# Performance work log

Hardware: AMD Instinct MI355X
Metric: run time of the kernel (lower is better)

## Reference

```python
import jax, jax.numpy as jnp
import numpy as np

SIGMA = 0.3
EPS = 1e-8  # torch CosineSimilarity eps
LOG_SQRT_2PI = float(0.5 * np.log(2.0 * np.pi))


def setup_inputs() -> dict:
    key = jax.random.key(0)
    k1, k2 = jax.random.split(key)
    Ex = jax.random.normal(k1, (8192, 256), dtype=jnp.float32)
    Ey = jax.random.normal(k2, (8192, 256), dtype=jnp.float32)
    return {"Ex": Ex, "Ey": Ey}


def reference(Ex, Ey):
    # cosine similarity: normalize rows (clamped norms), then dot -> [n, m]
    xn = Ex / jnp.maximum(jnp.linalg.norm(Ex, axis=-1, keepdims=True), EPS)
    yn = Ey / jnp.maximum(jnp.linalg.norm(Ey, axis=-1, keepdims=True), EPS)
    M = jnp.einsum('nd,md->nm', xn, yn)
    # Normal(loc=1, scale=sigma).log_prob
    z = (M - 1.0) / SIGMA
    logp = -0.5 * z * z - jnp.log(jnp.asarray(SIGMA, M.dtype)) - LOG_SQRT_2PI
    # C = -(exp(logp) * logp); row-wise min over y-tokens -> [n]
    C = -jnp.exp(logp) * logp
    return jnp.min(C, axis=-1)
```

## Files before the change

kernel.cpp:

```cpp
#include <hip/hip_runtime.h>
#include <hip/hip_bf16.h>

typedef unsigned short u16;
typedef __attribute__((ext_vector_type(8))) short short8;
typedef __attribute__((ext_vector_type(4))) float floatx4;

#define NROWS 8192
#define DIM 256

__device__ __forceinline__ void atomicMinFloat(float* addr, float val) {
    if (val >= 0.0f) {
        atomicMin((int*)addr, __float_as_int(val));
    } else {
        atomicMax((unsigned int*)addr, __float_as_uint(val));
    }
}

__device__ __forceinline__ u16 f32_to_bf16_rne(float x) {
    unsigned int u = __float_as_uint(x);
    unsigned int r = (u + 0x7fffu + ((u >> 16) & 1u)) >> 16;
    return (u16)r;
}

__device__ __forceinline__ float c_of_m(float m) {
    const float INV_SIG = 1.0f / 0.3f;
    const float KC = 0.28503427f;
    float z = (m - 1.0f) * INV_SIG;
    float logp = fmaf(-0.5f * z, z, KC);
    return -logp * __expf(logp);
}

__device__ __forceinline__ void load16(const u16* g, u16* l) {
    __builtin_amdgcn_global_load_lds(
        (__attribute__((address_space(1))) void*)g,
        (__attribute__((address_space(3))) void*)l, 16, 0, 0);
}

__global__ __launch_bounds__(256) void normalize_kernel(const float* __restrict__ Ex,
                                                        const float* __restrict__ Ey,
                                                        u16* __restrict__ Xs,
                                                        u16* __restrict__ Ys,
                                                        float* __restrict__ out) {
    const int t = threadIdx.x;
    const int ln = t & 63;
    const int row = blockIdx.x * 4 + (t >> 6);
    const float* src = (blockIdx.y == 0) ? Ex : Ey;
    u16* dst = (blockIdx.y == 0) ? Xs : Ys;

    float4 v = *(const float4*)(src + (size_t)row * DIM + ln * 4);
    float s = fmaf(v.x, v.x, fmaf(v.y, v.y, fmaf(v.z, v.z, v.w * v.w)));
    #pragma unroll
    for (int m = 32; m >= 1; m >>= 1) s += __shfl_xor(s, m, 64);
    float inv = 1.0f / fmaxf(sqrtf(s), 1e-8f);

    ushort4 o;
    o.x = f32_to_bf16_rne(v.x * inv);
    o.y = f32_to_bf16_rne(v.y * inv);
    o.z = f32_to_bf16_rne(v.z * inv);
    o.w = f32_to_bf16_rne(v.w * inv);

    const int p = row >> 4;
    const int lm = row & 15;
    const int kt = ln >> 3;
    const int lq = (ln >> 1) & 3;
    const int j4 = (ln & 1) * 4;
    const size_t off = ((size_t)((p * 8 + kt) * 64 + lq * 16 + lm)) * 8 + j4;
    *(ushort4*)(dst + off) = o;

    if (blockIdx.y == 0 && ln == 0) out[row] = __uint_as_float(0x7f800000u);
}

__global__ void __launch_bounds__(512, 2)
gemm_min_kernel(const u16* __restrict__ Xs,
                const u16* __restrict__ Ys,
                float* __restrict__ out) {
    __shared__ u16 Bs[2][16 * 512];

    const int tid = threadIdx.x;
    const int w = tid >> 6;
    const int lane = tid & 63;
    const int lq = lane >> 4;
    const int lm = lane & 15;

    const int i = blockIdx.x;
    const int x = i & 7;
    const int jj = i >> 3;
    const int rt = (x & 3) * 4 + (jj & 3);
    const int cgrp = (x >> 2) * 8 + (jj >> 2);

    const int rowStart = rt * 512;
    const int rowPan0 = rt * 32 + w * 4;
    const u16* ybase = Ys + (size_t)cgrp * 32 * 4096;

    auto stage1 = [&](int buf, const u16* yb, int iu) {
        const int u = w * 2 + iu;
        load16(yb + (u >> 3) * 4096 + (u & 7) * 512 + lane * 8,
               &Bs[buf][u * 512]);
    };

    short8 a[4][8];
    auto loadA = [&](int kt) {
        #pragma unroll
        for (int rg = 0; rg < 4; ++rg)
            a[rg][kt] = *(const short8*)(
                Xs + ((size_t)(rowPan0 + rg) * 8 + kt) * 512 + lane * 8);
    };

    floatx4 mn4[4], mx4[4];
    #pragma unroll
    for (int rg = 0; rg < 4; ++rg) {
        mn4[rg] = (floatx4){3.4e38f, 3.4e38f, 3.4e38f, 3.4e38f};
        mx4[rg] = (floatx4){-3.4e38f, -3.4e38f, -3.4e38f, -3.4e38f};
    }

    floatx4 acc[4][2];
    const floatx4 FZ = (floatx4){0.0f, 0.0f, 0.0f, 0.0f};

    auto compute = [&](int buf) {
        #pragma unroll
        for (int kt = 0; kt < 8; ++kt) {
            short8 bf[2];
            #pragma unroll
            for (int cg = 0; cg < 2; ++cg)
                bf[cg] = *(const short8*)(&Bs[buf][(cg * 8 + kt) * 512 + lane * 8]);
            if (kt == 0) {
                #pragma unroll
                for (int cg = 0; cg < 2; ++cg)
                    #pragma unroll
                    for (int rg = 0; rg < 4; ++rg)
                        acc[rg][cg] = __builtin_amdgcn_mfma_f32_16x16x32_bf16(
                            a[rg][0], bf[cg], FZ, 0, 0, 0);
            } else {
                #pragma unroll
                for (int cg = 0; cg < 2; ++cg)
                    #pragma unroll
                    for (int rg = 0; rg < 4; ++rg)
                        acc[rg][cg] = __builtin_amdgcn_mfma_f32_16x16x32_bf16(
                            a[rg][kt], bf[cg], acc[rg][cg], 0, 0, 0);
            }
        }
    };
    auto fold = [&]() {
        #pragma unroll
        for (int rg = 0; rg < 4; ++rg)
            #pragma unroll
            for (int cg = 0; cg < 2; ++cg)
                #pragma unroll
                for (int r = 0; r < 4; ++r) {
                    float m = acc[rg][cg][r];
                    mn4[rg][r] = fminf(mn4[rg][r], m);
                    mx4[rg][r] = fmaxf(mx4[rg][r], m);
                }
    };

    stage1(0, ybase, 0); stage1(0, ybase, 1);
    loadA(0); loadA(1);
    __syncthreads();
    stage1(1, ybase + 8192, 0); stage1(1, ybase + 8192, 1);
    loadA(2); loadA(3); loadA(4); loadA(5); loadA(6); loadA(7);
    compute(0);
    fold();
    ybase += 8192;

    #pragma unroll 1
    for (int ct = 1; ct < 16; ++ct) {
        const int buf = ct & 1;
        __syncthreads();
        if (ct < 15)
            stage1(buf ^ 1, ybase + 8192, 0), stage1(buf ^ 1, ybase + 8192, 1);
        compute(buf);
        fold();
        ybase += 8192;
    }

    #pragma unroll
    for (int rg = 0; rg < 4; ++rg) {
        #pragma unroll
        for (int r = 0; r < 4; ++r) {
            float mn = mn4[rg][r];
            float mx = mx4[rg][r];
            #pragma unroll
            for (int mofs = 1; mofs < 16; mofs <<= 1) {
                mn = fminf(mn, __shfl_xor(mn, mofs, 64));
                mx = fmaxf(mx, __shfl_xor(mx, mofs, 64));
            }
            if (lm == 0) {
                float cmin = fminf(c_of_m(mn), c_of_m(mx));
                int row = rowStart + w * 64 + rg * 16 + lq * 4 + r;
                atomicMinFloat(&out[row], cmin);
            }
        }
    }
}

extern "C" void kernel_launch(void* const* d_in, const int* in_sizes, int n_in,
                              void* d_out, int out_size, void* d_ws, size_t ws_size,
                              hipStream_t stream) {
    const float* Ex = (const float*)d_in[0];
    const float* Ey = (const float*)d_in[1];
    float* out = (float*)d_out;
    u16* Xs = (u16*)d_ws;
    u16* Ys = Xs + (size_t)NROWS * DIM;

    hipLaunchKernelGGL(normalize_kernel, dim3(NROWS / 4, 2), dim3(256), 0, stream,
                       Ex, Ey, Xs, Ys, out);
    hipLaunchKernelGGL(gemm_min_kernel, dim3(16 * 16), dim3(512), 0, stream,
                       Xs, Ys, out);
}
```

Baseline: 94.52 us.

## Rotate per-wave k-order and software-pipeline LDS B reads across tiles

Each wave now stages the Y k-slices it will consume first and walks the k dimension in a rotated order (w+s), so its first B fragments come from its own global-to-LDS loads. B fragments are double-buffered in registers and read from LDS one step ahead of the MFMAs. The first fragment of the next tile is read before the barrier, right after a vmcnt(0) wait on the wave's own staged loads. The fold of the previous tile's accumulators is moved into the start of the next compute to overlap with the LDS reads. The intent is to hide LDS latency and barrier stalls, at the cost of more registers and a subtle reliance on each wave having staged its own slices.

```diff
diff --git a/kernel.cpp b/kernel.cpp
--- a/kernel.cpp
+++ b/kernel.cpp
@@ -92,17 +92,17 @@
     const int rowPan0 = rt * 32 + w * 4;
     const u16* ybase = Ys + (size_t)cgrp * 32 * 4096;
 
-    auto stage1 = [&](int buf, const u16* yb, int iu) {
-        const int u = w * 2 + iu;
-        load16(yb + (u >> 3) * 4096 + (u & 7) * 512 + lane * 8,
-               &Bs[buf][u * 512]);
+    auto stageOwn = [&](int buf, const u16* yb) {
+        load16(yb + 0 * 4096 + w * 512 + lane * 8, &Bs[buf][(0 * 8 + w) * 512]);
+        load16(yb + 1 * 4096 + w * 512 + lane * 8, &Bs[buf][(8 + w) * 512]);
     };
 
     short8 a[4][8];
-    auto loadA = [&](int kt) {
+    auto loadA = [&](int s) {
+        const int kt = (w + s) & 7;
         #pragma unroll
         for (int rg = 0; rg < 4; ++rg)
-            a[rg][kt] = *(const short8*)(
+            a[rg][s] = *(const short8*)(
                 Xs + ((size_t)(rowPan0 + rg) * 8 + kt) * 512 + lane * 8);
     };
 
@@ -115,31 +115,8 @@
 
     floatx4 acc[4][2];
     const floatx4 FZ = (floatx4){0.0f, 0.0f, 0.0f, 0.0f};
-
-    auto compute = [&](int buf) {
-        #pragma unroll
-        for (int kt = 0; kt < 8; ++kt) {
-            short8 bf[2];
-            #pragma unroll
-            for (int cg = 0; cg < 2; ++cg)
-                bf[cg] = *(const short8*)(&Bs[buf][(cg * 8 + kt) * 512 + lane * 8]);
-            if (kt == 0) {
-                #pragma unroll
-                for (int cg = 0; cg < 2; ++cg)
-                    #pragma unroll
-                    for (int rg = 0; rg < 4; ++rg)
-                        acc[rg][cg] = __builtin_amdgcn_mfma_f32_16x16x32_bf16(
-                            a[rg][0], bf[cg], FZ, 0, 0, 0);
-            } else {
-                #pragma unroll
-                for (int cg = 0; cg < 2; ++cg)
-                    #pragma unroll
-                    for (int rg = 0; rg < 4; ++rg)
-                        acc[rg][cg] = __builtin_amdgcn_mfma_f32_16x16x32_bf16(
-                            a[rg][kt], bf[cg], acc[rg][cg], 0, 0, 0);
-            }
-        }
-    };
+    short8 bfA[2], bfB[2];
+
     auto fold = [&]() {
         #pragma unroll
         for (int rg = 0; rg < 4; ++rg)
@@ -153,13 +130,58 @@
                 }
     };
 
-    stage1(0, ybase, 0); stage1(0, ybase, 1);
+    auto compute = [&](int buf, bool PRE, bool dofold, bool doPrefetch) {
+        const u16* bsb = &Bs[buf][0];
+        auto rdB = [&](short8* dst, int s) {
+            const int kt = (w + s) & 7;
+            dst[0] = *(const short8*)(bsb + (0 * 8 + kt) * 512 + lane * 8);
+            dst[1] = *(const short8*)(bsb + (8 + kt) * 512 + lane * 8);
+        };
+        if (!PRE) rdB(bfA, 0);
+        rdB(bfB, 1);
+        if (dofold) fold();
+        #pragma unroll
+        for (int s2 = 0; s2 < 4; ++s2) {
+            const int se = 2 * s2;
+            const int so = se + 1;
+            if (se == 0) {
+                #pragma unroll
+                for (int cg = 0; cg < 2; ++cg)
+                    #pragma unroll
+                    for (int rg = 0; rg < 4; ++rg)
+                        acc[rg][cg] = __builtin_amdgcn_mfma_f32_16x16x32_bf16(
+                            a[rg][0], bfA[cg], FZ, 0, 0, 0);
+            } else {
+                #pragma unroll
+                for (int cg = 0; cg < 2; ++cg)
+                    #pragma unroll
+                    for (int rg = 0; rg < 4; ++rg)
+                        acc[rg][cg] = __builtin_amdgcn_mfma_f32_16x16x32_bf16(
+                            a[rg][se], bfA[cg], acc[rg][cg], 0, 0, 0);
+            }
+            if (se + 2 < 8) rdB(bfA, se + 2);
+            #pragma unroll
+            for (int cg = 0; cg < 2; ++cg)
+                #pragma unroll
+                for (int rg = 0; rg < 4; ++rg)
+                    acc[rg][cg] = __builtin_amdgcn_mfma_f32_16x16x32_bf16(
+                        a[rg][so], bfB[cg], acc[rg][cg], 0, 0, 0);
+            if (so + 2 < 8) rdB(bfB, so + 2);
+        }
+        if (doPrefetch) {
+            asm volatile("s_waitcnt vmcnt(0)" ::: "memory");
+            const u16* bnb = &Bs[buf ^ 1][0];
+            bfA[0] = *(const short8*)(bnb + (0 * 8 + w) * 512 + lane * 8);
+            bfA[1] = *(const short8*)(bnb + (8 + w) * 512 + lane * 8);
+        }
+    };
+
+    stageOwn(0, ybase);
     loadA(0); loadA(1);
     __syncthreads();
-    stage1(1, ybase + 8192, 0); stage1(1, ybase + 8192, 1);
+    stageOwn(1, ybase + 8192);
     loadA(2); loadA(3); loadA(4); loadA(5); loadA(6); loadA(7);
-    compute(0);
-    fold();
+    compute(0, false, false, true);
     ybase += 8192;
 
     #pragma unroll 1
@@ -167,11 +189,11 @@
         const int buf = ct & 1;
         __syncthreads();
         if (ct < 15)
-            stage1(buf ^ 1, ybase + 8192, 0), stage1(buf ^ 1, ybase + 8192, 1);
-        compute(buf);
-        fold();
+            stageOwn(buf ^ 1, ybase + 8192);
+        compute(buf, true, true, ct < 15);
         ybase += 8192;
     }
+    fold();
 
     #pragma unroll
     for (int rg = 0; rg < 4; ++rg) {
```

Measured after the change: 102.8 us. +8.7%, slower.

## Switch GEMM to 32x32x16 MFMA with matching operand layout and pipelined B reads

Applied to the files above, without the earlier changes.

Repacks the normalized bf16 operands into 32-row panels and replaces the 16x16x32 MFMA tiles with 32x32x16 MFMA, two row groups by one column group per wave over 16 k-steps. B fragments are read from LDS three steps ahead in a rotating register buffer. The min/max fold of the previous tile is moved inside the next compute call so it can overlap the MFMA chain. The cost targeted is LDS reads and instruction issue per FLOP. The final reduction needs more shuffle steps across 32 lanes.

```diff
diff --git a/kernel.cpp b/kernel.cpp
--- a/kernel.cpp
+++ b/kernel.cpp
@@ -3,7 +3,7 @@
 
 typedef unsigned short u16;
 typedef __attribute__((ext_vector_type(8))) short short8;
-typedef __attribute__((ext_vector_type(4))) float floatx4;
+typedef __attribute__((ext_vector_type(16))) float floatx16;
 
 #define NROWS 8192
 #define DIM 256
@@ -59,12 +59,12 @@
     o.z = f32_to_bf16_rne(v.z * inv);
     o.w = f32_to_bf16_rne(v.w * inv);
 
-    const int p = row >> 4;
-    const int lm = row & 15;
-    const int kt = ln >> 3;
-    const int lq = (ln >> 1) & 3;
-    const int j4 = (ln & 1) * 4;
-    const size_t off = ((size_t)((p * 8 + kt) * 64 + lq * 16 + lm)) * 8 + j4;
+    const int p32 = row >> 5;
+    const int rr = row & 31;
+    const int kt = ln >> 2;
+    const int half = (ln >> 1) & 1;
+    const int j0 = (ln & 1) * 4;
+    const size_t off = ((size_t)(p32 * 16 + kt) * 64 + half * 32 + rr) * 8 + j0;
     *(ushort4*)(dst + off) = o;
 
     if (blockIdx.y == 0 && ln == 0) out[row] = __uint_as_float(0x7f800000u);
@@ -79,8 +79,6 @@
     const int tid = threadIdx.x;
     const int w = tid >> 6;
     const int lane = tid & 63;
-    const int lq = lane >> 4;
-    const int lm = lane & 15;
 
     const int i = blockIdx.x;
     const int x = i & 7;
@@ -89,77 +87,78 @@
     const int cgrp = (x >> 2) * 8 + (jj >> 2);
 
     const int rowStart = rt * 512;
-    const int rowPan0 = rt * 32 + w * 4;
-    const u16* ybase = Ys + (size_t)cgrp * 32 * 4096;
+    const int p32A = rt * 16 + w * 2;
+    const u16* ybase = Ys + (size_t)cgrp * 16 * 8192;
 
     auto stage1 = [&](int buf, const u16* yb, int iu) {
         const int u = w * 2 + iu;
-        load16(yb + (u >> 3) * 4096 + (u & 7) * 512 + lane * 8,
-               &Bs[buf][u * 512]);
-    };
-
-    short8 a[4][8];
+        load16(yb + u * 512 + lane * 8, &Bs[buf][u * 512]);
+    };
+
+    short8 a[2][16];
     auto loadA = [&](int kt) {
         #pragma unroll
-        for (int rg = 0; rg < 4; ++rg)
+        for (int rg = 0; rg < 2; ++rg)
             a[rg][kt] = *(const short8*)(
-                Xs + ((size_t)(rowPan0 + rg) * 8 + kt) * 512 + lane * 8);
-    };
-
-    floatx4 mn4[4], mx4[4];
+                Xs + ((size_t)(p32A + rg) * 16 + kt) * 512 + lane * 8);
+    };
+
+    floatx16 mnv[2], mxv[2];
     #pragma unroll
-    for (int rg = 0; rg < 4; ++rg) {
-        mn4[rg] = (floatx4){3.4e38f, 3.4e38f, 3.4e38f, 3.4e38f};
-        mx4[rg] = (floatx4){-3.4e38f, -3.4e38f, -3.4e38f, -3.4e38f};
-    }
-
-    floatx4 acc[4][2];
-    const floatx4 FZ = (floatx4){0.0f, 0.0f, 0.0f, 0.0f};
-
-    auto compute = [&](int buf) {
-        #pragma unroll
-        for (int kt = 0; kt < 8; ++kt) {
-            short8 bf[2];
+    for (int rg = 0; rg < 2; ++rg)
+        #pragma unroll
+        for (int r = 0; r < 16; ++r) {
+            mnv[rg][r] = 3.4e38f;
+            mxv[rg][r] = -3.4e38f;
+        }
+
+    floatx16 acc[2];
+    const floatx16 FZ16 = (floatx16)(0.0f);
+
+    auto fold = [&]() {
+        #pragma unroll
+        for (int rg = 0; rg < 2; ++rg)
             #pragma unroll
-            for (int cg = 0; cg < 2; ++cg)
-                bf[cg] = *(const short8*)(&Bs[buf][(cg * 8 + kt) * 512 + lane * 8]);
+            for (int r = 0; r < 16; ++r) {
+                float m = acc[rg][r];
+                mnv[rg][r] = fminf(mnv[rg][r], m);
+                mxv[rg][r] = fmaxf(mxv[rg][r], m);
+            }
+    };
+
+    auto compute = [&](int buf, int dofold) {
+        const u16* bsb = &Bs[buf][0];
+        auto rdB = [&](int kt) {
+            return *(const short8*)(bsb + kt * 512 + lane * 8);
+        };
+        short8 bf[4];
+        bf[0] = rdB(0); bf[1] = rdB(1); bf[2] = rdB(2);
+        if (dofold) fold();
+        #pragma unroll
+        for (int kt = 0; kt < 16; ++kt) {
+            if (kt + 3 < 16) bf[(kt + 3) & 3] = rdB(kt + 3);
             if (kt == 0) {
-                #pragma unroll
-                for (int cg = 0; cg < 2; ++cg)
-                    #pragma unroll
-                    for (int rg = 0; rg < 4; ++rg)
-                        acc[rg][cg] = __builtin_amdgcn_mfma_f32_16x16x32_bf16(
-                            a[rg][0], bf[cg], FZ, 0, 0, 0);
+                acc[0] = __builtin_amdgcn_mfma_f32_32x32x16_bf16(
+                    a[0][0], bf[0], FZ16, 0, 0, 0);
+                acc[1] = __builtin_amdgcn_mfma_f32_32x32x16_bf16(
+                    a[1][0], bf[0], FZ16, 0, 0, 0);
             } else {
-                #pragma unroll
-                for (int cg = 0; cg < 2; ++cg)
-                    #pragma unroll
-                    for (int rg = 0; rg < 4; ++rg)
-                        acc[rg][cg] = __builtin_amdgcn_mfma_f32_16x16x32_bf16(
-                            a[rg][kt], bf[cg], acc[rg][cg], 0, 0, 0);
+                acc[0] = __builtin_amdgcn_mfma_f32_32x32x16_bf16(
+                    a[0][kt], bf[kt & 3], acc[0], 0, 0, 0);
+                acc[1] = __builtin_amdgcn_mfma_f32_32x32x16_bf16(
+                    a[1][kt], bf[kt & 3], acc[1], 0, 0, 0);
             }
         }
     };
-    auto fold = [&]() {
-        #pragma unroll
-        for (int rg = 0; rg < 4; ++rg)
-            #pragma unroll
-            for (int cg = 0; cg < 2; ++cg)
-                #pragma unroll
-                for (int r = 0; r < 4; ++r) {
-                    float m = acc[rg][cg][r];
-                    mn4[rg][r] = fminf(mn4[rg][r], m);
-                    mx4[rg][r] = fmaxf(mx4[rg][r], m);
-                }
-    };
 
     stage1(0, ybase, 0); stage1(0, ybase, 1);
-    loadA(0); loadA(1);
+    loadA(0); loadA(1); loadA(2); loadA(3);
     __syncthreads();
     stage1(1, ybase + 8192, 0); stage1(1, ybase + 8192, 1);
-    loadA(2); loadA(3); loadA(4); loadA(5); loadA(6); loadA(7);
-    compute(0);
-    fold();
+    loadA(4); loadA(5); loadA(6); loadA(7);
+    loadA(8); loadA(9); loadA(10); loadA(11);
+    loadA(12); loadA(13); loadA(14); loadA(15);
+    compute(0, 0);
     ybase += 8192;
 
     #pragma unroll 1
@@ -168,25 +167,26 @@
         __syncthreads();
         if (ct < 15)
             stage1(buf ^ 1, ybase + 8192, 0), stage1(buf ^ 1, ybase + 8192, 1);
-        compute(buf);
-        fold();
+        compute(buf, 1);
         ybase += 8192;
     }
+    fold();
 
     #pragma unroll
-    for (int rg = 0; rg < 4; ++rg) {
-        #pragma unroll
-        for (int r = 0; r < 4; ++r) {
-            float mn = mn4[rg][r];
-            float mx = mx4[rg][r];
+    for (int rg = 0; rg < 2; ++rg) {
+        #pragma unroll
+        for (int r = 0; r < 16; ++r) {
+            float mn = mnv[rg][r];
+            float mx = mxv[rg][r];
             #pragma unroll
-            for (int mofs = 1; mofs < 16; mofs <<= 1) {
+            for (int mofs = 1; mofs < 32; mofs <<= 1) {
                 mn = fminf(mn, __shfl_xor(mn, mofs, 64));
                 mx = fmaxf(mx, __shfl_xor(mx, mofs, 64));
             }
-            if (lm == 0) {
+            if ((lane & 31) == 0) {
                 float cmin = fminf(c_of_m(mn), c_of_m(mx));
-                int row = rowStart + w * 64 + rg * 16 + lq * 4 + r;
+                int row = rowStart + w * 64 + rg * 32 +
+                          (r & 3) + 8 * (r >> 2) + 4 * (lane >> 5);
                 atomicMinFloat(&out[row], cmin);
             }
         }
```

Measured after the change: 106.3 us. 1.12x slower.
